# Performance work log

Hardware: AMD Instinct MI355X
Metric: run time of the kernel (lower is better)

## Reference

```python
import jax, jax.numpy as jnp
import numpy as np

B, S, H, NH, T = 128, 512, 768, 8, 20
HD = H // NH


def setup_inputs() -> dict:
    key = jax.random.key(0)
    ks = jax.random.split(key, 16)
    f32 = jnp.float32
    def W(i, *shape):
        return jax.random.normal(ks[i], shape, f32) * 0.02
    inp = {}
    inp["ehs"] = jax.random.normal(ks[0], (B, S, H), f32)
    inp["relevance"] = jax.random.uniform(ks[1], (B, 1), dtype=f32)
    inp["threshold"] = jnp.array([0.5], f32)
    # text_to_caption_proj: Linear, LeakyReLU, LayerNorm, Linear
    inp["tW1"] = W(2, H, H); inp["tb1"] = jnp.zeros((H,), f32)
    inp["tg"] = jnp.ones((H,), f32); inp["tbe"] = jnp.zeros((H,), f32)
    inp["tW2"] = W(3, H, H); inp["tb2"] = jnp.zeros((H,), f32)
    # image_to_caption_proj
    inp["iW1"] = W(4, H, H); inp["ib1"] = jnp.zeros((H,), f32)
    inp["ig"] = jnp.ones((H,), f32); inp["ibe"] = jnp.zeros((H,), f32)
    inp["iW2"] = W(5, H, H); inp["ib2"] = jnp.zeros((H,), f32)
    # nn.MultiheadAttention packed in_proj [3H,H] + out_proj [H,H], x2
    inp["taWin"] = W(6, 3 * H, H); inp["taBin"] = jnp.zeros((3 * H,), f32)
    inp["taWout"] = W(7, H, H); inp["taBout"] = jnp.zeros((H,), f32)
    inp["iaWin"] = W(8, 3 * H, H); inp["iaBin"] = jnp.zeros((3 * H,), f32)
    inp["iaWout"] = W(9, H, H); inp["iaBout"] = jnp.zeros((H,), f32)
    # length_adapter: Linear, LayerNorm, ReLU
    inp["laW"] = W(10, H, H); inp["laB"] = jnp.zeros((H,), f32)
    inp["laG"] = jnp.ones((H,), f32); inp["laBe"] = jnp.zeros((H,), f32)
    # quality_estimator: Linear(H,H/2), LayerNorm, ReLU, Linear(H/2,1), Sigmoid
    inp["qW1"] = W(11, H // 2, H); inp["qB1"] = jnp.zeros((H // 2,), f32)
    inp["qG"] = jnp.ones((H // 2,), f32); inp["qBe"] = jnp.zeros((H // 2,), f32)
    inp["qW2"] = W(12, 1, H // 2); inp["qB2"] = jnp.zeros((1,), f32)
    # masks: first half = text tokens, second half = image tokens; no valid
    # image caption => torch loop gives batch_max_length=0 => target_length=20
    pos = jnp.arange(S)
    inp["sentence_mask"] = jnp.tile((pos < S // 2).astype(jnp.int32)[None], (B, 1))
    inp["image_mask"] = jnp.tile((pos >= S // 2).astype(jnp.int32)[None], (B, 1))
    inp["image_caption_mask"] = jnp.zeros((B, S), jnp.int32)
    inp["image_caption_valid"] = jnp.zeros((B,), jnp.int32)
    return inp


def _ln(x, g, b, eps=1e-5):
    m = x.mean(-1, keepdims=True)
    v = ((x - m) ** 2).mean(-1, keepdims=True)
    return (x - m) / jnp.sqrt(v + eps) * g + b


def _mha(q, k, v, Win, bIn, Wout, bOut, key_pad):
    # torch nn.MultiheadAttention, batch_first=True
    Wq, Wk, Wv = jnp.split(Win, 3, axis=0)
    bq, bk, bv = jnp.split(bIn, 3, axis=0)
    def heads(x, Wp, bp):  # [B,L,H] -> [B,NH,L,HD]
        return (x @ Wp.T + bp).reshape(x.shape[0], x.shape[1], NH, HD).transpose(0, 2, 1, 3)
    qh, kh, vh = heads(q, Wq, bq), heads(k, Wk, bk), heads(v, Wv, bv)
    scores = jnp.einsum('bhqd,bhkd->bhqk', qh, kh) / jnp.sqrt(jnp.float32(HD))
    scores = jnp.where(key_pad[:, None, None, :], -1e9, scores)
    attn = jax.nn.softmax(scores, axis=-1)
    out = jnp.einsum('bhqk,bhkd->bhqd', attn, vh)
    out = out.transpose(0, 2, 1, 3).reshape(q.shape[0], q.shape[1], H)
    return out @ Wout.T + bOut


def _sinusoid_pe():
    # vectorized replacement of the scalar double for-loop
    pos = jnp.arange(T, dtype=jnp.float32)[:, None]            # [T,1]
    i = jnp.arange(0, H, 2, dtype=jnp.float32)                 # [H/2]
    ang = pos / (10000.0 ** (i / H))                           # [T,H/2]
    pe = jnp.zeros((T, H), jnp.float32)
    pe = pe.at[:, 0::2].set(jnp.sin(ang)).at[:, 1::2].set(jnp.cos(ang))
    return pe[None]  # [1,T,H]


def reference(ehs, relevance, threshold,
              tW1, tb1, tg, tbe, tW2, tb2,
              iW1, ib1, ig, ibe, iW2, ib2,
              taWin, taBin, taWout, taBout,
              iaWin, iaBin, iaWout, iaBout,
              laW, laB, laG, laBe,
              qW1, qB1, qG, qBe, qW2, qB2,
              sentence_mask, image_mask, image_caption_mask, image_caption_valid):
    sm = sentence_mask.astype(jnp.float32)[..., None]   # [B,S,1]
    im = image_mask.astype(jnp.float32)[..., None]
    text_emb = ehs * sm
    image_emb = ehs * im
    # image_caption_valid is all False => target_length = min(20, max_length-2) = T (static)
    text_len = jnp.clip(sm.sum(axis=1), 1e-9)            # [B,1]
    img_len = jnp.clip(im.sum(axis=1), 1e-9)
    text_pooled = (text_emb * sm).sum(axis=1) / text_len  # mask applied twice, as in torch
    image_pooled = (image_emb * im).sum(axis=1) / img_len
    def proj(x, W1, b1, g, be, W2, b2):
        h = jax.nn.leaky_relu(x @ W1.T + b1, 0.01)
        return _ln(h, g, be) @ W2.T + b2
    text_seed = proj(text_pooled, tW1, tb1, tg, tbe, tW2, tb2)
    image_seed = proj(image_pooled, iW1, ib1, ig, ibe, iW2, ib2)
    alpha = relevance                                     # relevance_score provided
    caption_seed = alpha * image_seed + (1.0 - alpha) * text_seed
    query = caption_seed[:, None, :] + _sinusoid_pe()     # [B,T,H]
    text_cap = _mha(query, text_emb, text_emb, taWin, taBin, taWout, taBout, sentence_mask == 0)
    image_cap = _mha(query, image_emb, image_emb, iaWin, iaBin, iaWout, iaBout, image_mask == 0)
    beta = relevance[:, :, None]                          # [B,1,1]
    cap = beta * image_cap + (1.0 - beta) * text_cap
    cap = jax.nn.relu(_ln(cap @ laW.T + laB, laG, laBe))  # length_adapter
    m = cap.mean(axis=1)
    h = jax.nn.relu(_ln(m @ qW1.T + qB1, qG, qBe))
    quality = jax.nn.sigmoid(h @ qW2.T + qB2)             # [B,1]
    return cap, quality
```

## Files before the change

kernel.cpp:

```cpp
#include <hip/hip_runtime.h>
#include <hip/hip_bf16.h>
#include <math.h>

#define B_  128
#define S_  512
#define H_  768
#define NH_ 8
#define T_  20
#define HD_ 96

typedef unsigned short u16;
typedef unsigned int   u32;

typedef __attribute__((ext_vector_type(8))) short bhalf8;
typedef __attribute__((ext_vector_type(4))) float f32x4;

union U8 { bhalf8 s; u32 u[4]; };

__device__ __forceinline__ f32x4 mfma16(bhalf8 a, bhalf8 b, f32x4 c){
  return __builtin_amdgcn_mfma_f32_16x16x32_bf16(a, b, c, 0, 0, 0);
}
__device__ __forceinline__ u32 cvtpk(float lo, float hi){
  u32 r; asm volatile("v_cvt_pk_bf16_f32 %0, %1, %2" : "=v"(r) : "v"(lo), "v"(hi));
  return r;
}
__device__ __forceinline__ float wsum(float v){
  #pragma unroll
  for(int o=32;o;o>>=1) v += __shfl_xor(v,o);
  return v;
}
__device__ __forceinline__ u16 f2bf(float f){
  u32 u = __float_as_uint(f);
  u32 r = (u + 0x7fffu + ((u>>16)&1u)) >> 16;
  return (u16)r;
}
__device__ __forceinline__ float bf2f(u32 bits){
  return __uint_as_float(bits<<16);
}

__global__ void k_cvt(const float* __restrict__ src, u16* __restrict__ dst, int n2){
  int i = blockIdx.x*256 + threadIdx.x;
  if(i < n2){
    u32 r = cvtpk(src[2*i], src[2*i+1]);
    *(u32*)(dst + 2*i) = r;
  }
}

__global__ __launch_bounds__(256) void k_prep(const float* __restrict__ ehs,
                                              u16* __restrict__ ehs_b,
                                              u16* __restrict__ ehsT){
  int blk = blockIdx.x;
  int b  = blk / 96;
  int r  = blk % 96;
  int sb = r / 12, hb = r % 12;
  int s0 = sb*64, h0 = hb*64;
  __shared__ float tile[64][65];
  int t = threadIdx.x;
  const float* src = ehs + ((size_t)b*S_ + s0)*H_ + h0;
  #pragma unroll
  for(int p2=0;p2<4;p2++){
    int row = p2*16 + (t>>4);
    int c4  = (t&15)*4;
    float4 v = *(const float4*)(src + (size_t)row*H_ + c4);
    tile[row][c4+0]=v.x; tile[row][c4+1]=v.y; tile[row][c4+2]=v.z; tile[row][c4+3]=v.w;
    u32 lo = cvtpk(v.x, v.y), hi2 = cvtpk(v.z, v.w);
    u32* dst = (u32*)(ehs_b + ((size_t)b*S_ + s0 + row)*H_ + h0 + c4);
    dst[0]=lo; dst[1]=hi2;
  }
  __syncthreads();
  #pragma unroll
  for(int p2=0;p2<4;p2++){
    int hr = p2*16 + (t>>4);
    int sg = (t&15)*4;
    float a0 = tile[sg+0][hr], a1 = tile[sg+1][hr];
    float a2 = tile[sg+2][hr], a3 = tile[sg+3][hr];
    u32 lo = cvtpk(a0,a1), hi2 = cvtpk(a2,a3);
    u32* dst = (u32*)(ehsT + ((size_t)b*H_ + h0 + hr)*S_ + s0 + sg);
    dst[0]=lo; dst[1]=hi2;
  }
}

__global__ void k_wkt(const float* __restrict__ taWin, const float* __restrict__ iaWin,
                      u16* __restrict__ WkT){
  int blk = blockIdx.x; int mha = blk/576; int t = blk%576;
  const float* Wk = (mha? iaWin : taWin) + (size_t)H_*H_;
  int bx = t%24, by = t/24;
  __shared__ float tile[32][33];
  int tx = threadIdx.x & 31, ty = threadIdx.x >> 5;
  for(int rr=ty; rr<32; rr+=8) tile[rr][tx] = Wk[(size_t)(by*32+rr)*H_ + bx*32+tx];
  __syncthreads();
  u16* dst = WkT + (size_t)mha*H_*H_;
  for(int rr=ty; rr<32; rr+=8) dst[(size_t)(bx*32+rr)*H_ + by*32+tx] = f2bf(tile[tx][rr]);
}

__global__ void k_pool(const u16* __restrict__ ehs_b, const int* __restrict__ sm,
                       const int* __restrict__ im, u16* __restrict__ pt_b, u16* __restrict__ pi_b){
  int blk = blockIdx.x; int b = blk/3; int c0 = (blk%3)*256;
  int tid = threadIdx.x;
  __shared__ float smf[S_], imf[S_];
  for(int s=tid;s<S_;s+=256){ smf[s]=(float)sm[b*S_+s]; imf[s]=(float)im[b*S_+s]; }
  __syncthreads();
  float tl=0.f, il=0.f;
  for(int s=0;s<S_;s++){ tl+=smf[s]; il+=imf[s]; }
  tl = fmaxf(tl, 1e-9f); il = fmaxf(il, 1e-9f);
  int col = c0 + tid;
  const u16* base = ehs_b + (size_t)b*S_*H_ + col;
  float ts=0.f, is=0.f;
  for(int s=0;s<S_;s++){
    float a = bf2f(base[(size_t)s*H_]);
    ts += a*smf[s];
    is += a*imf[s];
  }
  pt_b[b*H_+col] = f2bf(ts/tl);
  pi_b[b*H_+col] = f2bf(is/il);
}

__global__ __launch_bounds__(512) void k_seed(const u16* __restrict__ x_b,
                                              const u16* __restrict__ W1_b,
                                              const float* __restrict__ b1,
                                              const float* __restrict__ g,
                                              const float* __restrict__ be,
                                              const u16* __restrict__ W2_b,
                                              const float* __restrict__ b2,
                                              float* __restrict__ out){
  int row0 = blockIdx.x*16;
  int tid = threadIdx.x, lane = tid&63, w = tid>>6;
  __shared__ u16 ln[16][772];
  f32x4 acc[6];
  #pragma unroll
  for(int j=0;j<6;j++) acc[j] = (f32x4){0.f,0.f,0.f,0.f};
  for(int kt=0;kt<24;kt++){
    int ko = kt*32 + (lane>>4)*8;
    bhalf8 a = *(const bhalf8*)(x_b + (size_t)(row0 + (lane&15))*H_ + ko);
    bhalf8 bb[6];
    #pragma unroll
    for(int j=0;j<6;j++){
      int row = (w*6+j)*16 + (lane&15);
      bb[j] = *(const bhalf8*)(W1_b + (size_t)row*H_ + ko);
    }
    #pragma unroll
    for(int j=0;j<6;j++) acc[j] = mfma16(a, bb[j], acc[j]);
  }
  #pragma unroll
  for(int j=0;j<6;j++){
    int c = (w*6+j)*16 + (lane&15);
    float bv = b1[c];
    #pragma unroll
    for(int rr=0;rr<4;rr++){
      int r = (lane>>4)*4 + rr;
      float v = acc[j][rr] + bv;
      ln[r][c] = f2bf((v>=0.f)? v : 0.01f*v);
    }
  }
  __syncthreads();
  for(int ri=0; ri<2; ri++){
    int r = w*2 + ri;
    float v[12]; float s = 0.f;
    #pragma unroll
    for(int i=0;i<12;i++){ v[i] = bf2f(ln[r][lane + 64*i]); s += v[i]; }
    s = wsum(s);
    float mean = s/(float)H_;
    float pv = 0.f;
    #pragma unroll
    for(int i=0;i<12;i++){ float d = v[i]-mean; pv += d*d; }
    pv = wsum(pv);
    float rstd = rsqrtf(pv/(float)H_ + 1e-5f);
    #pragma unroll
    for(int i=0;i<12;i++){
      int c = lane + 64*i;
      ln[r][c] = f2bf((v[i]-mean)*rstd*g[c] + be[c]);
    }
  }
  __syncthreads();
  f32x4 o[6];
  #pragma unroll
  for(int j=0;j<6;j++) o[j] = (f32x4){0.f,0.f,0.f,0.f};
  for(int kt=0;kt<24;kt++){
    int ko = kt*32 + (lane>>4)*8;
    bhalf8 a = *(const bhalf8*)(&ln[lane&15][ko]);
    bhalf8 bb[6];
    #pragma unroll
    for(int j=0;j<6;j++){
      int row = (w*6+j)*16 + (lane&15);
      bb[j] = *(const bhalf8*)(W2_b + (size_t)row*H_ + ko);
    }
    #pragma unroll
    for(int j=0;j<6;j++) o[j] = mfma16(a, bb[j], o[j]);
  }
  #pragma unroll
  for(int j=0;j<6;j++){
    int c = (w*6+j)*16 + (lane&15);
    float bv = b2[c];
    #pragma unroll
    for(int rr=0;rr<4;rr++){
      int r = (lane>>4)*4 + rr;
      out[(size_t)(row0 + r)*H_ + c] = o[j][rr] + bv;
    }
  }
}

__global__ void k_query(const float* __restrict__ st, const float* __restrict__ si,
                        const float* __restrict__ rel, u16* __restrict__ query_b){
  int b = blockIdx.x; int tid = threadIdx.x;
  float a = rel[b];
  const float c = 9.210340371976184f/(float)H_;
  for(int t=0;t<32;t++){
    for(int h=tid;h<H_;h+=256){
      float val = 0.f;
      if(t < T_){
        float ang = (float)t * __expf(-(float)(h & ~1) * c);
        float pe  = (h&1)? __cosf(ang) : __sinf(ang);
        val = a*si[b*H_+h] + (1.f-a)*st[b*H_+h] + pe;
      }
      query_b[(size_t)b*32*H_ + t*H_ + h] = f2bf(val);
    }
  }
}

__global__ __launch_bounds__(512) void k_qh(const u16* __restrict__ query_b,
                                            const u16* __restrict__ Wq_b,
                                            const float* __restrict__ taBin,
                                            const float* __restrict__ iaBin,
                                            u16* __restrict__ qh_b){
  int gb = blockIdx.x; int b = gb>>1, mha = gb&1;
  int tid = threadIdx.x, lane = tid&63, w = tid>>6;
  const u16* Q  = query_b + (size_t)b*32*H_;
  const u16* Wq = Wq_b + (size_t)mha*H_*H_;
  const float* bIn = mha? iaBin : taBin;
  u16* out = qh_b + (size_t)gb*32*H_;
  f32x4 acc[2][6];
  #pragma unroll
  for(int i=0;i<2;i++)
    #pragma unroll
    for(int j=0;j<6;j++) acc[i][j] = (f32x4){0.f,0.f,0.f,0.f};
  for(int kt=0;kt<24;kt++){
    int ko = kt*32 + (lane>>4)*8;
    bhalf8 a[2];
    #pragma unroll
    for(int mt=0;mt<2;mt++)
      a[mt] = *(const bhalf8*)(Q + (size_t)(mt*16 + (lane&15))*H_ + ko);
    bhalf8 bb[6];
    #pragma unroll
    for(int j=0;j<6;j++){
      int row = (w*6+j)*16 + (lane&15);
      bb[j] = *(const bhalf8*)(Wq + (size_t)row*H_ + ko);
    }
    #pragma unroll
    for(int mt=0;mt<2;mt++)
      #pragma unroll
      for(int j=0;j<6;j++) acc[mt][j] = mfma16(a[mt], bb[j], acc[mt][j]);
  }
  #pragma unroll
  for(int mt=0;mt<2;mt++)
    #pragma unroll
    for(int j=0;j<6;j++){
      int col = (w*6+j)*16 + (lane&15);
      float bq = bIn[col];
      #pragma unroll
      for(int rr=0;rr<4;rr++){
        int row = mt*16 + (lane>>4)*4 + rr;
        out[(size_t)row*H_ + col] = f2bf(acc[mt][j][rr] + bq);
      }
    }
}

__global__ __launch_bounds__(512) void k_u(const u16* __restrict__ qh_b,
                                           const u16* __restrict__ WkT,
                                           const float* __restrict__ taBin,
                                           const float* __restrict__ iaBin,
                                           u16* __restrict__ U_b,
                                           float* __restrict__ bias_ws){
  int gb = blockIdx.x; int mha = gb&1;
  int tid = threadIdx.x, lane = tid&63, w = tid>>6;
  const u16* qh = qh_b + (size_t)gb*32*H_;
  const u16* Wk = WkT + (size_t)mha*H_*H_;
  u16* Up = U_b + (size_t)gb*160*H_;
  __shared__ u16 ut[20][776];
  const float rscale = 0.10206207261596577f;
  for(int h=0; h<8; h++){
    int hd0 = h*HD_;
    for(int jn=0; jn<6; jn++){
      int nb = (w*6+jn)*16 + (lane&15);
      bhalf8 bb[3];
      #pragma unroll
      for(int kt=0;kt<3;kt++)
        bb[kt] = *(const bhalf8*)(Wk + (size_t)nb*H_ + hd0 + kt*32 + (lane>>4)*8);
      #pragma unroll
      for(int mt=0; mt<2; mt++){
        bhalf8 a[3];
        #pragma unroll
        for(int kt=0;kt<3;kt++){
          int trow = mt*16 + (lane&15);
          a[kt] = *(const bhalf8*)(qh + (size_t)trow*H_ + hd0 + kt*32 + (lane>>4)*8);
        }
        f32x4 acc = (f32x4){0.f,0.f,0.f,0.f};
        #pragma unroll
        for(int kt=0;kt<3;kt++) acc = mfma16(a[kt], bb[kt], acc);
        #pragma unroll
        for(int rr=0;rr<4;rr++){
          int trow = mt*16 + (lane>>4)*4 + rr;
          if(trow < T_)
            ut[trow][nb] = f2bf(acc[rr]*rscale);
        }
      }
    }
    __syncthreads();
    for(int e=tid; e<20*384; e+=512){
      int r = e/384, c2 = (e%384)*2;
      u32 v = *(const u32*)&ut[r][c2];
      *(u32*)(Up + (size_t)(h*T_ + r)*H_ + c2) = v;
    }
    __syncthreads();
  }
  if(tid < 160){
    int h = tid/T_, t = tid%T_; int hd0 = h*HD_;
    const float* bIn = mha? iaBin : taBin;
    float p = 0.f;
    for(int d=0; d<HD_; d++)
      p += bf2f(qh[(size_t)t*H_ + hd0 + d]) * bIn[H_ + hd0 + d];
    bias_ws[gb*160 + tid] = p*rscale;
  }
}

__global__ __launch_bounds__(512,4) void k_scores2(const u16* __restrict__ ehs_b,
                                                   const u16* __restrict__ U_b,
                                                   const float* __restrict__ bias_ws,
                                                   const int* __restrict__ smask,
                                                   const int* __restrict__ imask,
                                                   u16* __restrict__ P_b){
  int g = blockIdx.x;
  int x = g & 7, sl = g >> 3;
  int b = x*16 + (sl>>2);
  int var = sl & 3; int mha = var>>1, rhalf = var&1;
  int gb = 2*b + mha;
  const int* msk = mha? imask : smask;
  int tid = threadIdx.x, lane = tid&63, w = tid>>6;
  int rbase = rhalf*80;
  __shared__ float sbias[80];
  __shared__ float pmax[80][8];
  __shared__ float psum[80][8];
  __shared__ float mfin[80], sinv[80];
  __shared__ u16 pst[16][520];
  if(tid < 80) sbias[tid] = bias_ws[gb*160 + rbase + tid];
  __syncthreads();
  const u16* Ub = U_b + (size_t)gb*160*H_;
  const u16* Eb = ehs_b + (size_t)b*S_*H_;
  bool mk[4];
  #pragma unroll
  for(int j=0;j<4;j++) mk[j] = msk[b*S_ + w*64 + j*16 + (lane&15)] != 0;

  f32x4 acc[5][4];
  #pragma unroll
  for(int i=0;i<5;i++)
    #pragma unroll
    for(int j=0;j<4;j++) acc[i][j] = (f32x4){0.f,0.f,0.f,0.f};
  for(int kt=0;kt<24;kt++){
    int ko = kt*32 + (lane>>4)*8;
    bhalf8 a[5];
    #pragma unroll
    for(int i=0;i<5;i++)
      a[i] = *(const bhalf8*)(Ub + (size_t)(rbase + i*16 + (lane&15))*H_ + ko);
    bhalf8 bb[4];
    #pragma unroll
    for(int j=0;j<4;j++)
      bb[j] = *(const bhalf8*)(Eb + (size_t)(w*64 + j*16 + (lane&15))*H_ + ko);
    #pragma unroll
    for(int i=0;i<5;i++)
      #pragma unroll
      for(int j=0;j<4;j++) acc[i][j] = mfma16(a[i], bb[j], acc[i][j]);
  }
  #pragma unroll
  for(int i=0;i<5;i++)
    #pragma unroll
    for(int rr=0;rr<4;rr++){
      int row = i*16 + (lane>>4)*4 + rr;
      float bias = sbias[row];
      float vmax = -3e38f;
      #pragma unroll
      for(int j=0;j<4;j++){
        float v = acc[i][j][rr] + bias;
        acc[i][j][rr] = v;
        if(mk[j]) vmax = fmaxf(vmax, v);
      }
      #pragma unroll
      for(int o=1;o<16;o<<=1) vmax = fmaxf(vmax, __shfl_xor(vmax,o));
      if((lane&15)==0) pmax[row][w] = vmax;
    }
  __syncthreads();
  if(tid < 80){
    float m = pmax[tid][0];
    #pragma unroll
    for(int ww=1;ww<8;ww++) m = fmaxf(m, pmax[tid][ww]);
    mfin[tid] = m;
  }
  __syncthreads();
  #pragma unroll
  for(int i=0;i<5;i++)
    #pragma unroll
    for(int rr=0;rr<4;rr++){
      int row = i*16 + (lane>>4)*4 + rr;
      float m = mfin[row];
      float ssum = 0.f;
      #pragma unroll
      for(int j=0;j<4;j++){
        float e = mk[j]? __expf(acc[i][j][rr] - m) : 0.f;
        acc[i][j][rr] = e;
        ssum += e;
      }
      #pragma unroll
      for(int o=1;o<16;o<<=1) ssum += __shfl_xor(ssum,o);
      if((lane&15)==0) psum[row][w] = ssum;
    }
  __syncthreads();
  if(tid < 80){
    float ss = 0.f;
    #pragma unroll
    for(int ww=0;ww<8;ww++) ss += psum[tid][ww];
    sinv[tid] = 1.f/ss;
  }
  __syncthreads();
  u16* Pp = P_b + (size_t)gb*160*S_ + (size_t)rbase*S_;
  for(int i=0;i<5;i++){
    #pragma unroll
    for(int rr=0;rr<4;rr++){
      int r16 = (lane>>4)*4 + rr;
      float inv = sinv[i*16 + r16];
      #pragma unroll
      for(int j=0;j<4;j++){
        int col = w*64 + j*16 + (lane&15);
        pst[r16][col] = f2bf(acc[i][j][rr]*inv);
      }
    }
    __syncthreads();
    for(int e=tid; e<16*256; e+=512){
      int r16 = e>>8, c = e&255;
      u32 v = *(const u32*)&pst[r16][2*c];
      *(u32*)(Pp + (size_t)(i*16 + r16)*S_ + 2*c) = v;
    }
    __syncthreads();
  }
}

__global__ __launch_bounds__(512) void k_ctx2(const u16* __restrict__ ehsT,
                                              const u16* __restrict__ P_b,
                                              u16* __restrict__ ctx_b){
  int g = blockIdx.x;
  int x = g & 7, sl = g >> 3;
  int b = x*16 + (sl>>2);
  int var = sl & 3; int nh = var>>1, mha = var&1;
  int tid = threadIdx.x, lane = tid&63, w = tid>>6;
  __shared__ u16 ct[80][392];
  int nbase = nh*384 + w*48;
  const u16* Pp = P_b + (size_t)(2*b+mha)*160*S_;
  f32x4 acc[10][3];
  #pragma unroll
  for(int i=0;i<10;i++)
    #pragma unroll
    for(int j=0;j<3;j++) acc[i][j] = (f32x4){0.f,0.f,0.f,0.f};
  for(int kt=0;kt<16;kt++){
    int ko = kt*32 + (lane>>4)*8;
    bhalf8 bb[3];
    #pragma unroll
    for(int t2=0;t2<3;t2++){
      int n = nbase + t2*16 + (lane&15);
      bb[t2] = *(const bhalf8*)(ehsT + ((size_t)b*H_ + n)*S_ + ko);
    }
    bhalf8 a[10];
    #pragma unroll
    for(int i=0;i<10;i++){
      int row = i*16 + (lane&15);
      a[i] = *(const bhalf8*)(Pp + (size_t)row*S_ + ko);
    }
    #pragma unroll
    for(int i=0;i<10;i++)
      #pragma unroll
      for(int t2=0;t2<3;t2++) acc[i][t2] = mfma16(a[i], bb[t2], acc[i][t2]);
  }
  u16* Cp = ctx_b + (size_t)(2*b+mha)*160*H_ + nh*384;
  #pragma unroll
  for(int half=0; half<2; half++){
    __syncthreads();
    #pragma unroll
    for(int i=0;i<5;i++)
      #pragma unroll
      for(int t2=0;t2<3;t2++)
        #pragma unroll
        for(int rr=0;rr<4;rr++){
          int rloc = i*16 + (lane>>4)*4 + rr;
          int cl = w*48 + t2*16 + (lane&15);
          ct[rloc][cl] = f2bf(acc[half*5+i][t2][rr]);
        }
    __syncthreads();
    for(int e=tid; e<80*192; e+=512){
      int r = e/192, c2 = (e%192)*2;
      u32 v = (u32)ct[r][c2] | ((u32)ct[r][c2+1]<<16);
      *(u32*)(Cp + (size_t)(half*80 + r)*H_ + c2) = v;
    }
  }
}

__global__ __launch_bounds__(512) void k_out(const u16* __restrict__ ctx_b,
                                             const u16* __restrict__ Wv_b,
                                             const u16* __restrict__ Wo_b,
                                             const float* __restrict__ taBin,
                                             const float* __restrict__ iaBin,
                                             float* __restrict__ out_t,
                                             float* __restrict__ out_i){
  int gb = blockIdx.x; int b = gb>>1, mha = gb&1;
  int tid = threadIdx.x, lane = tid&63, w = tid>>6;
  const float* bIn = mha? iaBin : taBin;
  const u16* Wv = Wv_b + (size_t)mha*H_*H_;
  const u16* Wo = Wo_b + (size_t)mha*H_*H_;
  const u16* Cp = ctx_b + (size_t)gb*160*H_;
  __shared__ u16 vt[32][784];
  int hd0 = w*HD_;
  {
    f32x4 acc[2][6];
    #pragma unroll
    for(int i=0;i<2;i++)
      #pragma unroll
      for(int j=0;j<6;j++) acc[i][j] = (f32x4){0.f,0.f,0.f,0.f};
    for(int kt=0;kt<24;kt++){
      int ko = kt*32 + (lane>>4)*8;
      bhalf8 a[2];
      #pragma unroll
      for(int mt=0;mt<2;mt++){
        int trow = mt*16 + (lane&15);
        a[mt] = *(const bhalf8*)(Cp + (size_t)(w*T_ + trow)*H_ + ko);
      }
      bhalf8 bb[6];
      #pragma unroll
      for(int j=0;j<6;j++){
        int row = hd0 + j*16 + (lane&15);
        bb[j] = *(const bhalf8*)(Wv + (size_t)row*H_ + ko);
      }
      #pragma unroll
      for(int mt=0;mt<2;mt++)
        #pragma unroll
        for(int j=0;j<6;j++) acc[mt][j] = mfma16(a[mt], bb[j], acc[mt][j]);
    }
    #pragma unroll
    for(int mt=0;mt<2;mt++)
      #pragma unroll
      for(int j=0;j<6;j++){
        int col = j*16 + (lane&15);
        float bv = bIn[2*H_ + hd0 + col];
        #pragma unroll
        for(int rr=0;rr<4;rr++){
          int trow = mt*16 + (lane>>4)*4 + rr;
          vt[trow][hd0 + col] = f2bf(acc[mt][j][rr] + bv);
        }
      }
  }
  __syncthreads();
  {
    f32x4 o[2][6];
    #pragma unroll
    for(int i=0;i<2;i++)
      #pragma unroll
      for(int j=0;j<6;j++) o[i][j] = (f32x4){0.f,0.f,0.f,0.f};
    for(int kt=0;kt<24;kt++){
      int ko = kt*32 + (lane>>4)*8;
      bhalf8 a[2];
      #pragma unroll
      for(int mt=0;mt<2;mt++)
        a[mt] = *(const bhalf8*)(&vt[mt*16 + (lane&15)][ko]);
      bhalf8 bb[6];
      #pragma unroll
      for(int j=0;j<6;j++){
        int row = (w*6+j)*16 + (lane&15);
        bb[j] = *(const bhalf8*)(Wo + (size_t)row*H_ + ko);
      }
      #pragma unroll
      for(int mt=0;mt<2;mt++)
        #pragma unroll
        for(int j=0;j<6;j++) o[mt][j] = mfma16(a[mt], bb[j], o[mt][j]);
    }
    float* op = (mha? out_i : out_t) + (size_t)b*T_*H_;
    #pragma unroll
    for(int mt=0;mt<2;mt++)
      #pragma unroll
      for(int j=0;j<6;j++){
        int col = (w*6+j)*16 + (lane&15);
        #pragma unroll
        for(int rr=0;rr<4;rr++){
          int trow = mt*16 + (lane>>4)*4 + rr;
          if(trow < T_) op[(size_t)trow*H_ + col] = o[mt][j][rr];
        }
      }
  }
}

__global__ __launch_bounds__(512) void k_cap3(const float* __restrict__ out_t,
                                              const float* __restrict__ out_i,
                                              const float* __restrict__ taBout,
                                              const float* __restrict__ iaBout,
                                              const float* __restrict__ rel,
                                              const u16* __restrict__ laW_b,
                                              const float* __restrict__ laB,
                                              const float* __restrict__ laG,
                                              const float* __restrict__ laBe,
                                              float* __restrict__ cap){
  int blk = blockIdx.x; int row0 = blk*16;
  int tid = threadIdx.x, lane = tid&63, w = tid>>6;
  __shared__ float sy[16][776];
  __shared__ float sbo[H_], sbi[H_];
  for(int j=tid;j<H_;j+=512){ sbo[j]=taBout[j]; sbi[j]=iaBout[j]; }
  __syncthreads();
  int arow = row0 + (lane&15);
  float beta = rel[arow/T_];
  f32x4 acc[6];
  #pragma unroll
  for(int j=0;j<6;j++) acc[j] = (f32x4){0.f,0.f,0.f,0.f};
  for(int kt=0;kt<24;kt++){
    int ko = kt*32 + (lane>>4)*8;
    const float* tp = out_t + (size_t)arow*H_ + ko;
    const float* ip = out_i + (size_t)arow*H_ + ko;
    float4 t0 = *(const float4*)tp, t1 = *(const float4*)(tp+4);
    float4 i0 = *(const float4*)ip, i1 = *(const float4*)(ip+4);
    float v[8];
    v[0] = beta*(i0.x+sbi[ko+0]) + (1.f-beta)*(t0.x+sbo[ko+0]);
    v[1] = beta*(i0.y+sbi[ko+1]) + (1.f-beta)*(t0.y+sbo[ko+1]);
    v[2] = beta*(i0.z+sbi[ko+2]) + (1.f-beta)*(t0.z+sbo[ko+2]);
    v[3] = beta*(i0.w+sbi[ko+3]) + (1.f-beta)*(t0.w+sbo[ko+3]);
    v[4] = beta*(i1.x+sbi[ko+4]) + (1.f-beta)*(t1.x+sbo[ko+4]);
    v[5] = beta*(i1.y+sbi[ko+5]) + (1.f-beta)*(t1.y+sbo[ko+5]);
    v[6] = beta*(i1.z+sbi[ko+6]) + (1.f-beta)*(t1.z+sbo[ko+6]);
    v[7] = beta*(i1.w+sbi[ko+7]) + (1.f-beta)*(t1.w+sbo[ko+7]);
    U8 u;
    u.u[0]=cvtpk(v[0],v[1]); u.u[1]=cvtpk(v[2],v[3]);
    u.u[2]=cvtpk(v[4],v[5]); u.u[3]=cvtpk(v[6],v[7]);
    bhalf8 a = u.s;
    bhalf8 bb[6];
    #pragma unroll
    for(int j=0;j<6;j++){
      int row = (w*6+j)*16 + (lane&15);
      bb[j] = *(const bhalf8*)(laW_b + (size_t)row*H_ + ko);
    }
    #pragma unroll
    for(int j=0;j<6;j++) acc[j] = mfma16(a, bb[j], acc[j]);
  }
  #pragma unroll
  for(int j=0;j<6;j++){
    int c = (w*6+j)*16 + (lane&15);
    float lb = laB[c];
    #pragma unroll
    for(int rr=0;rr<4;rr++){
      int r = (lane>>4)*4 + rr;
      sy[r][c] = acc[j][rr] + lb;
    }
  }
  __syncthreads();
  for(int ri=0; ri<2; ri++){
    int r = w*2 + ri;
    float v[12];
    float s = 0.f;
    #pragma unroll
    for(int i=0;i<12;i++){ v[i] = sy[r][lane + 64*i]; s += v[i]; }
    s = wsum(s);
    float mean = s/(float)H_;
    float pv = 0.f;
    #pragma unroll
    for(int i=0;i<12;i++){ float d = v[i]-mean; pv += d*d; }
    pv = wsum(pv);
    float rstd = rsqrtf(pv/(float)H_ + 1e-5f);
    float* cp = cap + (size_t)(row0 + r)*H_;
    #pragma unroll
    for(int i=0;i<12;i++){
      int c = lane + 64*i;
      float o = (v[i]-mean)*rstd*laG[c] + laBe[c];
      cp[c] = (o>0.f)? o : 0.f;
    }
  }
}

__global__ __launch_bounds__(512) void k_quality2(const float* __restrict__ cap,
                                                  const u16* __restrict__ qW1_b,
                                                  const float* __restrict__ qB1,
                                                  const float* __restrict__ qG,
                                                  const float* __restrict__ qBe,
                                                  const float* __restrict__ qW2,
                                                  const float* __restrict__ qB2,
                                                  float* __restrict__ outq){
  const int H2 = H_/2;
  int b0 = blockIdx.x*16;
  int tid = threadIdx.x, lane = tid&63, w = tid>>6;
  __shared__ u16 sm_a[16][772];
  __shared__ float sy[16][388];
  for(int e=tid; e<16*H_; e+=512){
    int r = e/H_, c = e%H_;
    const float* cp = cap + ((size_t)(b0+r)*T_)*H_ + c;
    float s = 0.f;
    #pragma unroll
    for(int t=0;t<T_;t++) s += cp[(size_t)t*H_];
    sm_a[r][c] = f2bf(s*(1.f/(float)T_));
  }
  __syncthreads();
  f32x4 acc[3];
  #pragma unroll
  for(int j=0;j<3;j++) acc[j] = (f32x4){0.f,0.f,0.f,0.f};
  for(int kt=0;kt<24;kt++){
    int ko = kt*32 + (lane>>4)*8;
    bhalf8 a = *(const bhalf8*)(&sm_a[lane&15][ko]);
    bhalf8 bb[3];
    #pragma unroll
    for(int j=0;j<3;j++){
      int row = (w*3+j)*16 + (lane&15);
      bb[j] = *(const bhalf8*)(qW1_b + (size_t)row*H_ + ko);
    }
    #pragma unroll
    for(int j=0;j<3;j++) acc[j] = mfma16(a, bb[j], acc[j]);
  }
  #pragma unroll
  for(int j=0;j<3;j++){
    int c = (w*3+j)*16 + (lane&15);
    float q1 = qB1[c];
    #pragma unroll
    for(int rr=0;rr<4;rr++){
      int r = (lane>>4)*4 + rr;
      sy[r][c] = acc[j][rr] + q1;
    }
  }
  __syncthreads();
  for(int ri=0; ri<2; ri++){
    int r = w*2 + ri;
    float v[6]; float s = 0.f;
    #pragma unroll
    for(int i=0;i<6;i++){ v[i] = sy[r][lane + 64*i]; s += v[i]; }
    s = wsum(s);
    float mean = s/(float)H2;
    float pv = 0.f;
    #pragma unroll
    for(int i=0;i<6;i++){ float d = v[i]-mean; pv += d*d; }
    pv = wsum(pv);
    float rstd = rsqrtf(pv/(float)H2 + 1e-5f);
    float dot = 0.f;
    #pragma unroll
    for(int i=0;i<6;i++){
      int c = lane + 64*i;
      float u = (v[i]-mean)*rstd*qG[c] + qBe[c];
      u = (u>0.f)? u : 0.f;
      dot += u*qW2[c];
    }
    dot = wsum(dot);
    if(lane==0){
      float z = dot + qB2[0];
      outq[b0+r] = 1.f/(1.f+__expf(-z));
    }
  }
}

extern "C" void kernel_launch(void* const* d_in, const int* in_sizes, int n_in,
                              void* d_out, int out_size, void* d_ws, size_t ws_size,
                              hipStream_t stream){
  const float* ehs    = (const float*)d_in[0];
  const float* rel    = (const float*)d_in[1];
  const float* tW1    = (const float*)d_in[3];
  const float* tb1    = (const float*)d_in[4];
  const float* tg     = (const float*)d_in[5];
  const float* tbe    = (const float*)d_in[6];
  const float* tW2    = (const float*)d_in[7];
  const float* tb2    = (const float*)d_in[8];
  const float* iW1    = (const float*)d_in[9];
  const float* ib1    = (const float*)d_in[10];
  const float* ig     = (const float*)d_in[11];
  const float* ibe    = (const float*)d_in[12];
  const float* iW2    = (const float*)d_in[13];
  const float* ib2    = (const float*)d_in[14];
  const float* taWin  = (const float*)d_in[15];
  const float* taBin  = (const float*)d_in[16];
  const float* taWout = (const float*)d_in[17];
  const float* taBout = (const float*)d_in[18];
  const float* iaWin  = (const float*)d_in[19];
  const float* iaBin  = (const float*)d_in[20];
  const float* iaWout = (const float*)d_in[21];
  const float* iaBout = (const float*)d_in[22];
  const float* laW    = (const float*)d_in[23];
  const float* laB    = (const float*)d_in[24];
  const float* laG    = (const float*)d_in[25];
  const float* laBe   = (const float*)d_in[26];
  const float* qW1    = (const float*)d_in[27];
  const float* qB1    = (const float*)d_in[28];
  const float* qG     = (const float*)d_in[29];
  const float* qBe    = (const float*)d_in[30];
  const float* qW2    = (const float*)d_in[31];
  const float* qB2    = (const float*)d_in[32];
  const int* smask    = (const int*)d_in[33];
  const int* imask    = (const int*)d_in[34];

  char* p = (char*)d_ws;
  auto take = [&](size_t bytes)->char*{
    char* r = p; p += (bytes + 255) & ~(size_t)255; return r;
  };
  float* st      = (float*)take((size_t)B_*H_*4);
  float* si      = (float*)take((size_t)B_*H_*4);
  u16*  pt_b     = (u16*)take((size_t)B_*H_*2);
  u16*  pi_b     = (u16*)take((size_t)B_*H_*2);
  u16*  query_b  = (u16*)take((size_t)B_*32*H_*2);
  u16*  qh_b     = (u16*)take((size_t)B_*2*32*H_*2);
  u16*  WkT      = (u16*)take((size_t)2*H_*H_*2);
  u16*  Wq_b     = (u16*)take((size_t)2*H_*H_*2);
  u16*  Wv_b     = (u16*)take((size_t)2*H_*H_*2);
  u16*  Wo_b     = (u16*)take((size_t)2*H_*H_*2);
  u16*  laW_b    = (u16*)take((size_t)H_*H_*2);
  u16*  tW1_b    = (u16*)take((size_t)H_*H_*2);
  u16*  tW2_b    = (u16*)take((size_t)H_*H_*2);
  u16*  iW1_b    = (u16*)take((size_t)H_*H_*2);
  u16*  iW2_b    = (u16*)take((size_t)H_*H_*2);
  u16*  qW1_b    = (u16*)take((size_t)(H_/2)*H_*2);
  float* bias_ws = (float*)take((size_t)B_*2*160*4);
  u16*  U_b      = (u16*)take((size_t)B_*2*160*H_*2);
  u16*  P_b      = (u16*)take((size_t)B_*2*160*S_*2);
  float* out_t   = (float*)take((size_t)B_*T_*H_*4);
  float* out_i   = (float*)take((size_t)B_*T_*H_*4);
  u16*  ehs_b    = (u16*)take((size_t)B_*S_*H_*2);
  u16*  ehsT     = (u16*)take((size_t)B_*H_*S_*2);
  u16*  ctx_b    = U_b;

  const int nW2 = (H_*H_)/2;
  const int cvtg = (nW2 + 255)/256;
  const int nQ2 = ((H_/2)*H_)/2;
  const int cvtgq = (nQ2 + 255)/256;

  hipLaunchKernelGGL(k_prep, dim3(B_*96), dim3(256), 0, stream, ehs, ehs_b, ehsT);

  hipLaunchKernelGGL(k_cvt, dim3(cvtg), dim3(256), 0, stream, taWin,              Wq_b,           nW2);
  hipLaunchKernelGGL(k_cvt, dim3(cvtg), dim3(256), 0, stream, iaWin,              Wq_b + (size_t)H_*H_, nW2);
  hipLaunchKernelGGL(k_cvt, dim3(cvtg), dim3(256), 0, stream, taWin + 2*H_*H_,    Wv_b,           nW2);
  hipLaunchKernelGGL(k_cvt, dim3(cvtg), dim3(256), 0, stream, iaWin + 2*H_*H_,    Wv_b + (size_t)H_*H_, nW2);
  hipLaunchKernelGGL(k_cvt, dim3(cvtg), dim3(256), 0, stream, taWout,             Wo_b,           nW2);
  hipLaunchKernelGGL(k_cvt, dim3(cvtg), dim3(256), 0, stream, iaWout,             Wo_b + (size_t)H_*H_, nW2);
  hipLaunchKernelGGL(k_cvt, dim3(cvtg), dim3(256), 0, stream, laW,                laW_b,          nW2);
  hipLaunchKernelGGL(k_cvt, dim3(cvtg), dim3(256), 0, stream, tW1,                tW1_b,          nW2);
  hipLaunchKernelGGL(k_cvt, dim3(cvtg), dim3(256), 0, stream, tW2,                tW2_b,          nW2);
  hipLaunchKernelGGL(k_cvt, dim3(cvtg), dim3(256), 0, stream, iW1,                iW1_b,          nW2);
  hipLaunchKernelGGL(k_cvt, dim3(cvtg), dim3(256), 0, stream, iW2,                iW2_b,          nW2);
  hipLaunchKernelGGL(k_cvt, dim3(cvtgq), dim3(256), 0, stream, qW1,               qW1_b,          nQ2);
  hipLaunchKernelGGL(k_wkt, dim3(1152), dim3(256), 0, stream, taWin, iaWin, WkT);

  hipLaunchKernelGGL(k_pool,  dim3(B_*3), dim3(256), 0, stream, ehs_b, smask, imask, pt_b, pi_b);
  hipLaunchKernelGGL(k_seed,  dim3(B_/16), dim3(512), 0, stream, pt_b, tW1_b, tb1, tg, tbe, tW2_b, tb2, st);
  hipLaunchKernelGGL(k_seed,  dim3(B_/16), dim3(512), 0, stream, pi_b, iW1_b, ib1, ig, ibe, iW2_b, ib2, si);
  hipLaunchKernelGGL(k_query, dim3(B_),   dim3(256), 0, stream, st, si, rel, query_b);

  hipLaunchKernelGGL(k_qh,      dim3(B_*2),  dim3(512), 0, stream, query_b, Wq_b, taBin, iaBin, qh_b);
  hipLaunchKernelGGL(k_u,       dim3(B_*2),  dim3(512), 0, stream, qh_b, WkT, taBin, iaBin, U_b, bias_ws);
  hipLaunchKernelGGL(k_scores2, dim3(B_*4),  dim3(512), 0, stream, ehs_b, U_b, bias_ws, smask, imask, P_b);
  hipLaunchKernelGGL(k_ctx2,    dim3(B_*4),  dim3(512), 0, stream, ehsT, P_b, ctx_b);
  hipLaunchKernelGGL(k_out,     dim3(B_*2),  dim3(512), 0, stream, ctx_b, Wv_b, Wo_b, taBin, iaBin, out_t, out_i);

  float* cap = (float*)d_out;
  hipLaunchKernelGGL(k_cap3, dim3((B_*T_)/16), dim3(512), 0, stream,
                     out_t, out_i, taBout, iaBout, rel, laW_b, laB, laG, laBe, cap);
  hipLaunchKernelGGL(k_quality2, dim3(B_/16), dim3(512), 0, stream,
                     cap, qW1_b, qB1, qG, qBe, qW2, qB2, cap + (size_t)B_*T_*H_);
}
```

Before: 838.7 us.

## Merge weight conversions and seed projections into single launches; vectorize pooling

```diff
diff --git a/kernel.cpp b/kernel.cpp
--- a/kernel.cpp
+++ b/kernel.cpp
@@ -38,12 +38,23 @@
   return __uint_as_float(bits<<16);
 }
 
-__global__ void k_cvt(const float* __restrict__ src, u16* __restrict__ dst, int n2){
-  int i = blockIdx.x*256 + threadIdx.x;
-  if(i < n2){
-    u32 r = cvtpk(src[2*i], src[2*i+1]);
-    *(u32*)(dst + 2*i) = r;
-  }
+__global__ void k_cvtall(const float* __restrict__ s0, const float* __restrict__ s1,
+                         const float* __restrict__ s2, const float* __restrict__ s3,
+                         const float* __restrict__ s4, const float* __restrict__ s5,
+                         const float* __restrict__ s6, const float* __restrict__ s7,
+                         const float* __restrict__ s8, const float* __restrict__ s9,
+                         const float* __restrict__ s10, const float* __restrict__ s11,
+                         u16* __restrict__ dst){
+  const int NP = (H_*H_)/2;
+  int idx = blockIdx.x*256 + threadIdx.x;
+  int seg, po;
+  if(idx < 11*NP){ seg = idx / NP; po = idx - seg*NP; }
+  else           { seg = 11; po = idx - 11*NP; if(po >= NP/2) return; }
+  const float* src =
+    seg==0? s0 : seg==1? s1 : seg==2? s2 : seg==3? s3 : seg==4? s4 : seg==5? s5 :
+    seg==6? s6 : seg==7? s7 : seg==8? s8 : seg==9? s9 : seg==10? s10 : s11;
+  u32 r = cvtpk(src[2*po], src[2*po+1]);
+  *(u32*)(dst + (size_t)seg*(H_*H_) + 2*po) = r;
 }
 
 __global__ __launch_bounds__(256) void k_prep(const float* __restrict__ ehs,
@@ -93,37 +104,63 @@
   for(int rr=ty; rr<32; rr+=8) dst[(size_t)(bx*32+rr)*H_ + by*32+tx] = f2bf(tile[tx][rr]);
 }
 
-__global__ void k_pool(const u16* __restrict__ ehs_b, const int* __restrict__ sm,
-                       const int* __restrict__ im, u16* __restrict__ pt_b, u16* __restrict__ pi_b){
-  int blk = blockIdx.x; int b = blk/3; int c0 = (blk%3)*256;
-  int tid = threadIdx.x;
+__global__ __launch_bounds__(384) void k_pool2(const u16* __restrict__ ehs_b,
+                                               const int* __restrict__ sm,
+                                               const int* __restrict__ im,
+                                               u16* __restrict__ pt_b, u16* __restrict__ pi_b){
+  int b = blockIdx.x, tid = threadIdx.x;
   __shared__ float smf[S_], imf[S_];
-  for(int s=tid;s<S_;s+=256){ smf[s]=(float)sm[b*S_+s]; imf[s]=(float)im[b*S_+s]; }
+  __shared__ float part[2][4][96][8];
+  for(int s=tid;s<S_;s+=384){ smf[s]=(float)sm[b*S_+s]; imf[s]=(float)im[b*S_+s]; }
+  __syncthreads();
+  int hg = tid % 96, sp = tid / 96;
+  float ts[8], is[8];
+  #pragma unroll
+  for(int j=0;j<8;j++){ ts[j]=0.f; is[j]=0.f; }
+  for(int s=sp*128; s<sp*128+128; s++){
+    U8 u; u.s = *(const bhalf8*)(ehs_b + ((size_t)b*S_+s)*H_ + hg*8);
+    float mt = smf[s], mi = imf[s];
+    #pragma unroll
+    for(int j=0;j<4;j++){
+      float lo = bf2f(u.u[j]&0xffffu), hi = bf2f(u.u[j]>>16);
+      ts[2*j]   += lo*mt; ts[2*j+1] += hi*mt;
+      is[2*j]   += lo*mi; is[2*j+1] += hi*mi;
+    }
+  }
+  #pragma unroll
+  for(int j=0;j<8;j++){ part[0][sp][hg][j]=ts[j]; part[1][sp][hg][j]=is[j]; }
   __syncthreads();
   float tl=0.f, il=0.f;
   for(int s=0;s<S_;s++){ tl+=smf[s]; il+=imf[s]; }
   tl = fmaxf(tl, 1e-9f); il = fmaxf(il, 1e-9f);
-  int col = c0 + tid;
-  const u16* base = ehs_b + (size_t)b*S_*H_ + col;
-  float ts=0.f, is=0.f;
-  for(int s=0;s<S_;s++){
-    float a = bf2f(base[(size_t)s*H_]);
-    ts += a*smf[s];
-    is += a*imf[s];
-  }
-  pt_b[b*H_+col] = f2bf(ts/tl);
-  pi_b[b*H_+col] = f2bf(is/il);
-}
-
-__global__ __launch_bounds__(512) void k_seed(const u16* __restrict__ x_b,
-                                              const u16* __restrict__ W1_b,
-                                              const float* __restrict__ b1,
-                                              const float* __restrict__ g,
-                                              const float* __restrict__ be,
-                                              const u16* __restrict__ W2_b,
-                                              const float* __restrict__ b2,
-                                              float* __restrict__ out){
-  int row0 = blockIdx.x*16;
+  for(int e=tid; e<H_; e+=384){
+    int hg2 = e/8, j = e%8;
+    float t = part[0][0][hg2][j]+part[0][1][hg2][j]+part[0][2][hg2][j]+part[0][3][hg2][j];
+    float i2= part[1][0][hg2][j]+part[1][1][hg2][j]+part[1][2][hg2][j]+part[1][3][hg2][j];
+    pt_b[b*H_+e] = f2bf(t/tl);
+    pi_b[b*H_+e] = f2bf(i2/il);
+  }
+}
+
+__global__ __launch_bounds__(512) void k_seed2(const u16* __restrict__ pt_b,
+                                               const u16* __restrict__ pi_b,
+                                               const u16* __restrict__ tW1_b, const float* __restrict__ tb1,
+                                               const float* __restrict__ tg,  const float* __restrict__ tbe,
+                                               const u16* __restrict__ tW2_b, const float* __restrict__ tb2,
+                                               const u16* __restrict__ iW1_b, const float* __restrict__ ib1,
+                                               const float* __restrict__ ig,  const float* __restrict__ ibe,
+                                               const u16* __restrict__ iW2_b, const float* __restrict__ ib2,
+                                               float* __restrict__ st, float* __restrict__ si){
+  int which = blockIdx.x >= (B_/16);
+  int row0 = (blockIdx.x - which*(B_/16))*16;
+  const u16* x_b  = which? pi_b  : pt_b;
+  const u16* W1_b = which? iW1_b : tW1_b;
+  const float* b1 = which? ib1 : tb1;
+  const float* g  = which? ig  : tg;
+  const float* be = which? ibe : tbe;
+  const u16* W2_b = which? iW2_b : tW2_b;
+  const float* b2 = which? ib2 : tb2;
+  float* out      = which? si : st;
   int tid = threadIdx.x, lane = tid&63, w = tid>>6;
   __shared__ u16 ln[16][772];
   f32x4 acc[6];
@@ -817,31 +854,20 @@
   u16*  ehsT     = (u16*)take((size_t)B_*H_*S_*2);
   u16*  ctx_b    = U_b;
 
-  const int nW2 = (H_*H_)/2;
-  const int cvtg = (nW2 + 255)/256;
-  const int nQ2 = ((H_/2)*H_)/2;
-  const int cvtgq = (nQ2 + 255)/256;
-
   hipLaunchKernelGGL(k_prep, dim3(B_*96), dim3(256), 0, stream, ehs, ehs_b, ehsT);
 
-  hipLaunchKernelGGL(k_cvt, dim3(cvtg), dim3(256), 0, stream, taWin,              Wq_b,           nW2);
-  hipLaunchKernelGGL(k_cvt, dim3(cvtg), dim3(256), 0, stream, iaWin,              Wq_b + (size_t)H_*H_, nW2);
-  hipLaunchKernelGGL(k_cvt, dim3(cvtg), dim3(256), 0, stream, taWin + 2*H_*H_,    Wv_b,           nW2);
-  hipLaunchKernelGGL(k_cvt, dim3(cvtg), dim3(256), 0, stream, iaWin + 2*H_*H_,    Wv_b + (size_t)H_*H_, nW2);
-  hipLaunchKernelGGL(k_cvt, dim3(cvtg), dim3(256), 0, stream, taWout,             Wo_b,           nW2);
-  hipLaunchKernelGGL(k_cvt, dim3(cvtg), dim3(256), 0, stream, iaWout,             Wo_b + (size_t)H_*H_, nW2);
-  hipLaunchKernelGGL(k_cvt, dim3(cvtg), dim3(256), 0, stream, laW,                laW_b,          nW2);
-  hipLaunchKernelGGL(k_cvt, dim3(cvtg), dim3(256), 0, stream, tW1,                tW1_b,          nW2);
-  hipLaunchKernelGGL(k_cvt, dim3(cvtg), dim3(256), 0, stream, tW2,                tW2_b,          nW2);
-  hipLaunchKernelGGL(k_cvt, dim3(cvtg), dim3(256), 0, stream, iW1,                iW1_b,          nW2);
-  hipLaunchKernelGGL(k_cvt, dim3(cvtg), dim3(256), 0, stream, iW2,                iW2_b,          nW2);
-  hipLaunchKernelGGL(k_cvt, dim3(cvtgq), dim3(256), 0, stream, qW1,               qW1_b,          nQ2);
+  const int NP = (H_*H_)/2;
+  const int cvtallg = (11*NP + NP/2 + 255)/256;
+  hipLaunchKernelGGL(k_cvtall, dim3(cvtallg), dim3(256), 0, stream,
+                     taWin, iaWin, taWin + 2*H_*H_, iaWin + 2*H_*H_,
+                     taWout, iaWout, laW, tW1, tW2, iW1, iW2, qW1, Wq_b);
   hipLaunchKernelGGL(k_wkt, dim3(1152), dim3(256), 0, stream, taWin, iaWin, WkT);
 
-  hipLaunchKernelGGL(k_pool,  dim3(B_*3), dim3(256), 0, stream, ehs_b, smask, imask, pt_b, pi_b);
-  hipLaunchKernelGGL(k_seed,  dim3(B_/16), dim3(512), 0, stream, pt_b, tW1_b, tb1, tg, tbe, tW2_b, tb2, st);
-  hipLaunchKernelGGL(k_seed,  dim3(B_/16), dim3(512), 0, stream, pi_b, iW1_b, ib1, ig, ibe, iW2_b, ib2, si);
-  hipLaunchKernelGGL(k_query, dim3(B_),   dim3(256), 0, stream, st, si, rel, query_b);
+  hipLaunchKernelGGL(k_pool2, dim3(B_), dim3(384), 0, stream, ehs_b, smask, imask, pt_b, pi_b);
+  hipLaunchKernelGGL(k_seed2, dim3(B_/8), dim3(512), 0, stream,
+                     pt_b, pi_b, tW1_b, tb1, tg, tbe, tW2_b, tb2,
+                     iW1_b, ib1, ig, ibe, iW2_b, ib2, st, si);
+  hipLaunchKernelGGL(k_query, dim3(B_), dim3(256), 0, stream, st, si, rel, query_b);
 
   hipLaunchKernelGGL(k_qh,      dim3(B_*2),  dim3(512), 0, stream, query_b, Wq_b, taBin, iaBin, qh_b);
   hipLaunchKernelGGL(k_u,       dim3(B_*2),  dim3(512), 0, stream, qh_b, WkT, taBin, iaBin, U_b, bias_ws);
```

Result: faster. 749.0 us (-10.7%).
